# Kernel tuning notes

Hardware: AMD Instinct MI355X
Metric: run time of the kernel (lower is better)

## Reference

```python
import jax, jax.numpy as jnp
import numpy as np

ALPHA = 10.0   # args.alpha softmax sharpness
EPS = 1e-8     # torch CosineSimilarity eps


def setup_inputs() -> dict:
    key = jax.random.key(0)
    k0, k1, k2, k3 = jax.random.split(key, 4)
    B, S, F, D, C = 8, 1024, 32, 128, 16
    Hs = jax.random.normal(k0, (B, S, F, D), dtype=jnp.float32)
    Cj = jax.random.normal(k1, (C, D), dtype=jnp.float32)
    W = jax.random.normal(k2, (D, D), dtype=jnp.float32) * 0.05  # nn.Linear weight [out,in]
    b = jnp.zeros((D,), dtype=jnp.float32)
    importance = jax.random.uniform(k3, (B, S, F), dtype=jnp.float32)
    return {"Hs": Hs, "Cj": Cj, "W": W, "b": b, "importance": importance}


def reference(Hs, Cj, W, b, importance):
    # Hs: [B,S,F,D] features; Cj: [C,D] cluster centers; importance: [B,S,F]
    # Faithful to Model_DTSSOCC.assignment (importance is not None branch),
    # but avoids materializing the broadcasted [B,S,F,C,D] repeat tensors.
    Hn = Hs / jnp.maximum(jnp.linalg.norm(Hs, axis=-1, keepdims=True), EPS)
    Cn = Cj / jnp.maximum(jnp.linalg.norm(Cj, axis=-1, keepdims=True), EPS)
    cos = jnp.einsum('bsfd,cd->bsfc', Hn, Cn)            # cosine_sim4 over dim D
    logits = -ALPHA * 0.5 * (1.0 - cos)                  # -alpha * dists, [B,S,F,C]
    w3 = jax.nn.softmax(logits, axis=3)                  # softmax over centers
    w = jax.nn.softmax(logits, axis=2)                   # softmax over feas
    w3 = jnp.swapaxes(w3, 2, 3)                          # [B,S,C,F]
    w = jnp.swapaxes(w, 2, 3)                            # [B,S,C,F]
    F_tj = jax.nn.relu(jnp.einsum('bsfd,ed->bsfe', Hs, W) + b)  # relu(Linear(F_t))
    # importance update: bmm(w3, importance) then softmax over centers
    imp = jax.nn.softmax(jnp.einsum('bscf,bsf->bsc', w3, importance), axis=2)
    # weighted feature aggregation: bmm(w, F_tj) -> [B,S,C,D]
    f_t_new = jnp.einsum('bscf,bsfd->bscd', w, F_tj)
    return f_t_new, imp
```

## Files before the change

kernel.cpp:

```cpp
#include <hip/hip_runtime.h>
#include <hip/hip_bf16.h>
#include <math.h>

constexpr int Bn = 8, Sn = 1024, Fn = 32, Dn = 128, Cc = 16;
constexpr int NSITE = Bn * Sn;

#define EPSV 1e-8f

typedef __attribute__((ext_vector_type(8))) short bf16x8;
typedef __attribute__((ext_vector_type(4))) short bf16x4;
typedef __attribute__((ext_vector_type(4))) float f32x4;

__device__ inline short f2bf(float x) {
    __hip_bfloat16 h = __float2bfloat16(x);
    short s;
    __builtin_memcpy(&s, &h, sizeof(s));
    return s;
}

__device__ inline bf16x8 cvt8(f32x4 x0, f32x4 x1) {
    bf16x8 r;
    r[0] = f2bf(x0[0]); r[1] = f2bf(x0[1]); r[2] = f2bf(x0[2]); r[3] = f2bf(x0[3]);
    r[4] = f2bf(x1[0]); r[5] = f2bf(x1[1]); r[6] = f2bf(x1[2]); r[7] = f2bf(x1[3]);
    return r;
}

template<int CTRL>
__device__ __forceinline__ float dpp_add(float v) {
    union { float f; int i; } u, r;
    u.f = v;
    r.i = __builtin_amdgcn_update_dpp(0, u.i, CTRL, 0xf, 0xf, true);
    return v + r.f;
}
__device__ __forceinline__ float rowsum16(float v) {
    v = dpp_add<0x121>(v);
    v = dpp_add<0x122>(v);
    v = dpp_add<0x124>(v);
    v = dpp_add<0x128>(v);
    return v;
}
__device__ __forceinline__ float fastrcp(float x) { return __builtin_amdgcn_rcpf(x); }

__global__ void prep_kernel(const float* __restrict__ Cj,
                            const float* __restrict__ W,
                            short* __restrict__ CnPack,
                            short* __restrict__ Wb) {
    const int tid = threadIdx.x;
    if (blockIdx.x < 64) {
        int t = blockIdx.x * 256 + tid;
        int n = t >> 7, k = t & 127;
        short v = f2bf(W[n * Dn + k]);
        int frag = (n >> 4) * 4 + (k >> 5);
        int lane = ((k >> 3) & 3) * 16 + (n & 15);
        Wb[(frag * 64 + lane) * 8 + (k & 7)] = v;
    } else {
        int c = blockIdx.x - 64;
        __shared__ float part[2];
        float v = 0.f, sq = 0.f;
        if (tid < 128) {
            v = Cj[c * Dn + tid];
            sq = v * v;
            #pragma unroll
            for (int off = 32; off > 0; off >>= 1) sq += __shfl_down(sq, off);
        }
        if (tid < 128 && (tid & 63) == 0) part[tid >> 6] = sq;
        __syncthreads();
        if (tid < 128) {
            float cn = v / fmaxf(sqrtf(part[0] + part[1]), EPSV);
            int kt = tid >> 5, ln = ((tid >> 3) & 3) * 16 + c, j = tid & 7;
            CnPack[(kt * 64 + ln) * 8 + j] = f2bf(cn);
        }
    }
}

__launch_bounds__(64, 4)
__global__ void site_kernel(const float* __restrict__ Hs,
                            const short* __restrict__ CnPack,
                            const short* __restrict__ Wb,
                            const float* __restrict__ bvec,
                            const float* __restrict__ imp_in,
                            float* __restrict__ f_out,
                            float* __restrict__ imp_out) {
    __shared__ __align__(16) short F_tjT[128][40];
    __shared__ __align__(16) float sO[16][33];

    const int lane = threadIdx.x;
    const int c16  = lane & 15;
    const int g    = lane >> 4;
    const int site = blockIdx.x;

    const float* hsrc = Hs + (size_t)site * (Fn * Dn);
    const f32x4 zro = {0.f, 0.f, 0.f, 0.f};

    f32x4 x[16];
    #pragma unroll
    for (int kt = 0; kt < 4; ++kt) {
        const f32x4* p0 = (const f32x4*)(hsrc + c16 * Dn + kt * 32 + g * 8);
        const f32x4* p1 = (const f32x4*)(hsrc + (16 + c16) * Dn + kt * 32 + g * 8);
        x[4 * kt + 0] = p0[0];
        x[4 * kt + 1] = p0[1];
        x[4 * kt + 2] = p1[0];
        x[4 * kt + 3] = p1[1];
    }
    bf16x8 bcf[4];
    #pragma unroll
    for (int kt = 0; kt < 4; ++kt)
        bcf[kt] = *(const bf16x8*)&CnPack[(kt * 64 + lane) * 8];
    const float* impp = imp_in + (size_t)site * Fn;
    f32x4 impv0 = *(const f32x4*)(impp + 4 * g);
    f32x4 impv1 = *(const f32x4*)(impp + 16 + 4 * g);

    bf16x8 aF[2][4];
    #pragma unroll
    for (int kt = 0; kt < 4; ++kt) {
        aF[0][kt] = cvt8(x[4 * kt + 0], x[4 * kt + 1]);
        aF[1][kt] = cvt8(x[4 * kt + 2], x[4 * kt + 3]);
    }

    f32x4 gm0 = zro, gm1 = zro, cos0 = zro, cos1 = zro;
    #pragma unroll
    for (int kt = 0; kt < 4; ++kt) {
        gm0  = __builtin_amdgcn_mfma_f32_16x16x32_bf16(aF[0][kt], aF[0][kt], gm0, 0, 0, 0);
        gm1  = __builtin_amdgcn_mfma_f32_16x16x32_bf16(aF[1][kt], aF[1][kt], gm1, 0, 0, 0);
        cos0 = __builtin_amdgcn_mfma_f32_16x16x32_bf16(aF[0][kt], bcf[kt], cos0, 0, 0, 0);
        cos1 = __builtin_amdgcn_mfma_f32_16x16x32_bf16(aF[1][kt], bcf[kt], cos1, 0, 0, 0);
    }

    float e0[4], e1[4];
    #pragma unroll
    for (int r = 0; r < 4; ++r) {
        float q0 = __shfl(gm0[r], 20 * g + r);
        float q1 = __shfl(gm1[r], 20 * g + r);
        float i0 = fastrcp(fmaxf(sqrtf(q0), EPSV));
        float i1 = fastrcp(fmaxf(sqrtf(q1), EPSV));
        e0[r] = __expf(5.0f * cos0[r] * i0);
        e1[r] = __expf(5.0f * cos1[r] * i1);
    }

    bf16x8 wB;
    {
        float sum = 0.f;
        #pragma unroll
        for (int r = 0; r < 4; ++r) sum += e0[r] + e1[r];
        sum += __shfl_xor(sum, 16);
        sum += __shfl_xor(sum, 32);
        float inv = fastrcp(sum);
        const int srcA = c16 + 16 * ((2 * g) & 3);
        const int srcB = c16 + 16 * ((2 * g + 1) & 3);
        const bool hi = (g >= 2);
        #pragma unroll
        for (int r = 0; r < 4; ++r) {
            float a0 = __shfl(e0[r] * inv, srcA);
            float a1 = __shfl(e1[r] * inv, srcA);
            wB[r] = f2bf(hi ? a1 : a0);
            float b0 = __shfl(e0[r] * inv, srcB);
            float b1 = __shfl(e1[r] * inv, srcB);
            wB[4 + r] = f2bf(hi ? b1 : b0);
        }
    }

    {
        float t = 0.f;
        #pragma unroll
        for (int h = 0; h < 2; ++h) {
            #pragma unroll
            for (int r = 0; r < 4; ++r) {
                float e = h ? e1[r] : e0[r];
                float q3 = rowsum16(e);
                t += e * fastrcp(q3) * (h ? impv1[r] : impv0[r]);
            }
        }
        t += __shfl_xor(t, 16);
        t += __shfl_xor(t, 32);
        float ei = __expf(t);
        float si = rowsum16(ei);
        if (g == 0) imp_out[(size_t)site * Cc + c16] = ei * fastrcp(si);
    }

    #pragma unroll
    for (int nt = 0; nt < 8; ++nt) {
        bf16x8 bw0 = *(const bf16x8*)&Wb[((nt * 4) + 0) * 512 + lane * 8];
        bf16x8 bw1 = *(const bf16x8*)&Wb[((nt * 4) + 1) * 512 + lane * 8];
        bf16x8 bw2 = *(const bf16x8*)&Wb[((nt * 4) + 2) * 512 + lane * 8];
        bf16x8 bw3 = *(const bf16x8*)&Wb[((nt * 4) + 3) * 512 + lane * 8];
        f32x4 acc0 = zro, acc1 = zro;
        acc0 = __builtin_amdgcn_mfma_f32_16x16x32_bf16(aF[0][0], bw0, acc0, 0, 0, 0);
        acc1 = __builtin_amdgcn_mfma_f32_16x16x32_bf16(aF[1][0], bw0, acc1, 0, 0, 0);
        acc0 = __builtin_amdgcn_mfma_f32_16x16x32_bf16(aF[0][1], bw1, acc0, 0, 0, 0);
        acc1 = __builtin_amdgcn_mfma_f32_16x16x32_bf16(aF[1][1], bw1, acc1, 0, 0, 0);
        acc0 = __builtin_amdgcn_mfma_f32_16x16x32_bf16(aF[0][2], bw2, acc0, 0, 0, 0);
        acc1 = __builtin_amdgcn_mfma_f32_16x16x32_bf16(aF[1][2], bw2, acc1, 0, 0, 0);
        acc0 = __builtin_amdgcn_mfma_f32_16x16x32_bf16(aF[0][3], bw3, acc0, 0, 0, 0);
        acc1 = __builtin_amdgcn_mfma_f32_16x16x32_bf16(aF[1][3], bw3, acc1, 0, 0, 0);
        float bb = bvec[nt * 16 + c16];
        bf16x4 p0, p1;
        #pragma unroll
        for (int r = 0; r < 4; ++r) {
            p0[r] = f2bf(fmaxf(acc0[r] + bb, 0.f));
            p1[r] = f2bf(fmaxf(acc1[r] + bb, 0.f));
        }
        *(bf16x4*)&F_tjT[nt * 16 + c16][4 * g]      = p0;
        *(bf16x4*)&F_tjT[nt * 16 + c16][16 + 4 * g] = p1;
    }

    {
        float* op = f_out + (size_t)site * (Cc * Dn);
        #pragma unroll
        for (int p = 0; p < 4; ++p) {
            #pragma unroll
            for (int h = 0; h < 2; ++h) {
                const int nt = 2 * p + h;
                bf16x8 aFt = *(const bf16x8*)&F_tjT[nt * 16 + c16][8 * g];
                f32x4 o = __builtin_amdgcn_mfma_f32_16x16x32_bf16(aFt, wB, zro, 0, 0, 0);
                *(f32x4*)&sO[c16][h * 16 + 4 * g] = o;
            }
            #pragma unroll
            for (int i = 0; i < 2; ++i) {
                const int row = 8 * i + (lane >> 3);
                const int cir = lane & 7;
                f32x4 v = *(const f32x4*)&sO[row][cir * 4];
                *(f32x4*)(op + row * Dn + p * 32 + cir * 4) = v;
            }
        }
    }
}

extern "C" void kernel_launch(void* const* d_in, const int* in_sizes, int n_in,
                              void* d_out, int out_size, void* d_ws, size_t ws_size,
                              hipStream_t stream) {
    const float* Hs  = (const float*)d_in[0];
    const float* Cj  = (const float*)d_in[1];
    const float* W   = (const float*)d_in[2];
    const float* b   = (const float*)d_in[3];
    const float* imp = (const float*)d_in[4];

    float* f_out   = (float*)d_out;
    float* imp_out = f_out + (size_t)NSITE * Cc * Dn;

    short* CnPack = (short*)d_ws;
    short* Wb     = CnPack + Cc * Dn;

    hipLaunchKernelGGL(prep_kernel, dim3(80), dim3(256), 0, stream, Cj, W, CnPack, Wb);
    hipLaunchKernelGGL(site_kernel, dim3(NSITE), dim3(64), 0, stream,
                       Hs, CnPack, Wb, b, imp, f_out, imp_out);
}
```

Measured before the change: 44.63 us.

## Process two sites per wavefront with staggered loads of the second site

Each 64-thread block now handles two consecutive sites, launching half as many blocks. The second site's Hs loads are issued in two halves interleaved with the bf16 conversion of the first site, so more memory traffic is in flight per wave. The per-site compute is wrapped in a lambda and run sequentially for both sites. The extra register state for two sites is accommodated by lowering the launch-bounds occupancy hint from 4 to 3, which may reduce latency hiding across waves.

```diff
diff --git a/kernel.cpp b/kernel.cpp
--- a/kernel.cpp
+++ b/kernel.cpp
@@ -73,7 +73,7 @@
     }
 }
 
-__launch_bounds__(64, 4)
+__launch_bounds__(64, 3)
 __global__ void site_kernel(const float* __restrict__ Hs,
                             const short* __restrict__ CnPack,
                             const short* __restrict__ Wb,
@@ -87,142 +87,176 @@
     const int lane = threadIdx.x;
     const int c16  = lane & 15;
     const int g    = lane >> 4;
-    const int site = blockIdx.x;
-
-    const float* hsrc = Hs + (size_t)site * (Fn * Dn);
+    const int sA   = blockIdx.x * 2;
+    const int sB   = sA + 1;
+
+    const float* hA = Hs + (size_t)sA * (Fn * Dn);
+    const float* hB = Hs + (size_t)sB * (Fn * Dn);
     const f32x4 zro = {0.f, 0.f, 0.f, 0.f};
 
-    f32x4 x[16];
+    f32x4 xA[16], xB[16];
     #pragma unroll
     for (int kt = 0; kt < 4; ++kt) {
-        const f32x4* p0 = (const f32x4*)(hsrc + c16 * Dn + kt * 32 + g * 8);
-        const f32x4* p1 = (const f32x4*)(hsrc + (16 + c16) * Dn + kt * 32 + g * 8);
-        x[4 * kt + 0] = p0[0];
-        x[4 * kt + 1] = p0[1];
-        x[4 * kt + 2] = p1[0];
-        x[4 * kt + 3] = p1[1];
-    }
+        const f32x4* p0 = (const f32x4*)(hA + c16 * Dn + kt * 32 + g * 8);
+        const f32x4* p1 = (const f32x4*)(hA + (16 + c16) * Dn + kt * 32 + g * 8);
+        xA[4 * kt + 0] = p0[0];
+        xA[4 * kt + 1] = p0[1];
+        xA[4 * kt + 2] = p1[0];
+        xA[4 * kt + 3] = p1[1];
+    }
+    #pragma unroll
+    for (int kt = 0; kt < 2; ++kt) {
+        const f32x4* p0 = (const f32x4*)(hB + c16 * Dn + kt * 32 + g * 8);
+        const f32x4* p1 = (const f32x4*)(hB + (16 + c16) * Dn + kt * 32 + g * 8);
+        xB[4 * kt + 0] = p0[0];
+        xB[4 * kt + 1] = p0[1];
+        xB[4 * kt + 2] = p1[0];
+        xB[4 * kt + 3] = p1[1];
+    }
+    bf16x8 aFA[2][4], aFB[2][4];
+    #pragma unroll
+    for (int kt = 0; kt < 4; ++kt) {
+        aFA[0][kt] = cvt8(xA[4 * kt + 0], xA[4 * kt + 1]);
+        aFA[1][kt] = cvt8(xA[4 * kt + 2], xA[4 * kt + 3]);
+    }
+    #pragma unroll
+    for (int kt = 2; kt < 4; ++kt) {
+        const f32x4* p0 = (const f32x4*)(hB + c16 * Dn + kt * 32 + g * 8);
+        const f32x4* p1 = (const f32x4*)(hB + (16 + c16) * Dn + kt * 32 + g * 8);
+        xB[4 * kt + 0] = p0[0];
+        xB[4 * kt + 1] = p0[1];
+        xB[4 * kt + 2] = p1[0];
+        xB[4 * kt + 3] = p1[1];
+    }
+    #pragma unroll
+    for (int kt = 0; kt < 4; ++kt) {
+        aFB[0][kt] = cvt8(xB[4 * kt + 0], xB[4 * kt + 1]);
+        aFB[1][kt] = cvt8(xB[4 * kt + 2], xB[4 * kt + 3]);
+    }
+
     bf16x8 bcf[4];
     #pragma unroll
     for (int kt = 0; kt < 4; ++kt)
         bcf[kt] = *(const bf16x8*)&CnPack[(kt * 64 + lane) * 8];
-    const float* impp = imp_in + (size_t)site * Fn;
-    f32x4 impv0 = *(const f32x4*)(impp + 4 * g);
-    f32x4 impv1 = *(const f32x4*)(impp + 16 + 4 * g);
-
-    bf16x8 aF[2][4];
-    #pragma unroll
-    for (int kt = 0; kt < 4; ++kt) {
-        aF[0][kt] = cvt8(x[4 * kt + 0], x[4 * kt + 1]);
-        aF[1][kt] = cvt8(x[4 * kt + 2], x[4 * kt + 3]);
-    }
-
-    f32x4 gm0 = zro, gm1 = zro, cos0 = zro, cos1 = zro;
-    #pragma unroll
-    for (int kt = 0; kt < 4; ++kt) {
-        gm0  = __builtin_amdgcn_mfma_f32_16x16x32_bf16(aF[0][kt], aF[0][kt], gm0, 0, 0, 0);
-        gm1  = __builtin_amdgcn_mfma_f32_16x16x32_bf16(aF[1][kt], aF[1][kt], gm1, 0, 0, 0);
-        cos0 = __builtin_amdgcn_mfma_f32_16x16x32_bf16(aF[0][kt], bcf[kt], cos0, 0, 0, 0);
-        cos1 = __builtin_amdgcn_mfma_f32_16x16x32_bf16(aF[1][kt], bcf[kt], cos1, 0, 0, 0);
-    }
-
-    float e0[4], e1[4];
-    #pragma unroll
-    for (int r = 0; r < 4; ++r) {
-        float q0 = __shfl(gm0[r], 20 * g + r);
-        float q1 = __shfl(gm1[r], 20 * g + r);
-        float i0 = fastrcp(fmaxf(sqrtf(q0), EPSV));
-        float i1 = fastrcp(fmaxf(sqrtf(q1), EPSV));
-        e0[r] = __expf(5.0f * cos0[r] * i0);
-        e1[r] = __expf(5.0f * cos1[r] * i1);
-    }
-
-    bf16x8 wB;
-    {
-        float sum = 0.f;
+    const float* impA = imp_in + (size_t)sA * Fn;
+    const float* impB = imp_in + (size_t)sB * Fn;
+    f32x4 impA0 = *(const f32x4*)(impA + 4 * g);
+    f32x4 impA1 = *(const f32x4*)(impA + 16 + 4 * g);
+    f32x4 impB0 = *(const f32x4*)(impB + 4 * g);
+    f32x4 impB1 = *(const f32x4*)(impB + 16 + 4 * g);
+
+    auto run_site = [&](int site, const bf16x8 (&aF)[2][4],
+                        const f32x4& impv0, const f32x4& impv1) {
+        f32x4 gm0 = zro, gm1 = zro, cos0 = zro, cos1 = zro;
         #pragma unroll
-        for (int r = 0; r < 4; ++r) sum += e0[r] + e1[r];
-        sum += __shfl_xor(sum, 16);
-        sum += __shfl_xor(sum, 32);
-        float inv = fastrcp(sum);
-        const int srcA = c16 + 16 * ((2 * g) & 3);
-        const int srcB = c16 + 16 * ((2 * g + 1) & 3);
-        const bool hi = (g >= 2);
+        for (int kt = 0; kt < 4; ++kt) {
+            gm0  = __builtin_amdgcn_mfma_f32_16x16x32_bf16(aF[0][kt], aF[0][kt], gm0, 0, 0, 0);
+            gm1  = __builtin_amdgcn_mfma_f32_16x16x32_bf16(aF[1][kt], aF[1][kt], gm1, 0, 0, 0);
+            cos0 = __builtin_amdgcn_mfma_f32_16x16x32_bf16(aF[0][kt], bcf[kt], cos0, 0, 0, 0);
+            cos1 = __builtin_amdgcn_mfma_f32_16x16x32_bf16(aF[1][kt], bcf[kt], cos1, 0, 0, 0);
+        }
+
+        float e0[4], e1[4];
         #pragma unroll
         for (int r = 0; r < 4; ++r) {
-            float a0 = __shfl(e0[r] * inv, srcA);
-            float a1 = __shfl(e1[r] * inv, srcA);
-            wB[r] = f2bf(hi ? a1 : a0);
-            float b0 = __shfl(e0[r] * inv, srcB);
-            float b1 = __shfl(e1[r] * inv, srcB);
-            wB[4 + r] = f2bf(hi ? b1 : b0);
-        }
-    }
-
-    {
-        float t = 0.f;
+            float q0 = __shfl(gm0[r], 20 * g + r);
+            float q1 = __shfl(gm1[r], 20 * g + r);
+            float i0 = fastrcp(fmaxf(sqrtf(q0), EPSV));
+            float i1 = fastrcp(fmaxf(sqrtf(q1), EPSV));
+            e0[r] = __expf(5.0f * cos0[r] * i0);
+            e1[r] = __expf(5.0f * cos1[r] * i1);
+        }
+
+        bf16x8 wB;
+        {
+            float sum = 0.f;
+            #pragma unroll
+            for (int r = 0; r < 4; ++r) sum += e0[r] + e1[r];
+            sum += __shfl_xor(sum, 16);
+            sum += __shfl_xor(sum, 32);
+            float inv = fastrcp(sum);
+            const int srcA = c16 + 16 * ((2 * g) & 3);
+            const int srcB = c16 + 16 * ((2 * g + 1) & 3);
+            const bool hi = (g >= 2);
+            #pragma unroll
+            for (int r = 0; r < 4; ++r) {
+                float a0 = __shfl(e0[r] * inv, srcA);
+                float a1 = __shfl(e1[r] * inv, srcA);
+                wB[r] = f2bf(hi ? a1 : a0);
+                float b0 = __shfl(e0[r] * inv, srcB);
+                float b1 = __shfl(e1[r] * inv, srcB);
+                wB[4 + r] = f2bf(hi ? b1 : b0);
+            }
+        }
+
+        {
+            float t = 0.f;
+            #pragma unroll
+            for (int h = 0; h < 2; ++h) {
+                #pragma unroll
+                for (int r = 0; r < 4; ++r) {
+                    float e = h ? e1[r] : e0[r];
+                    float q3 = rowsum16(e);
+                    t += e * fastrcp(q3) * (h ? impv1[r] : impv0[r]);
+                }
+            }
+            t += __shfl_xor(t, 16);
+            t += __shfl_xor(t, 32);
+            float ei = __expf(t);
+            float si = rowsum16(ei);
+            if (g == 0) imp_out[(size_t)site * Cc + c16] = ei * fastrcp(si);
+        }
+
         #pragma unroll
-        for (int h = 0; h < 2; ++h) {
+        for (int nt = 0; nt < 8; ++nt) {
+            bf16x8 bw0 = *(const bf16x8*)&Wb[((nt * 4) + 0) * 512 + lane * 8];
+            bf16x8 bw1 = *(const bf16x8*)&Wb[((nt * 4) + 1) * 512 + lane * 8];
+            bf16x8 bw2 = *(const bf16x8*)&Wb[((nt * 4) + 2) * 512 + lane * 8];
+            bf16x8 bw3 = *(const bf16x8*)&Wb[((nt * 4) + 3) * 512 + lane * 8];
+            f32x4 acc0 = zro, acc1 = zro;
+            acc0 = __builtin_amdgcn_mfma_f32_16x16x32_bf16(aF[0][0], bw0, acc0, 0, 0, 0);
+            acc1 = __builtin_amdgcn_mfma_f32_16x16x32_bf16(aF[1][0], bw0, acc1, 0, 0, 0);
+            acc0 = __builtin_amdgcn_mfma_f32_16x16x32_bf16(aF[0][1], bw1, acc0, 0, 0, 0);
+            acc1 = __builtin_amdgcn_mfma_f32_16x16x32_bf16(aF[1][1], bw1, acc1, 0, 0, 0);
+            acc0 = __builtin_amdgcn_mfma_f32_16x16x32_bf16(aF[0][2], bw2, acc0, 0, 0, 0);
+            acc1 = __builtin_amdgcn_mfma_f32_16x16x32_bf16(aF[1][2], bw2, acc1, 0, 0, 0);
+            acc0 = __builtin_amdgcn_mfma_f32_16x16x32_bf16(aF[0][3], bw3, acc0, 0, 0, 0);
+            acc1 = __builtin_amdgcn_mfma_f32_16x16x32_bf16(aF[1][3], bw3, acc1, 0, 0, 0);
+            float bb = bvec[nt * 16 + c16];
+            bf16x4 p0, p1;
             #pragma unroll
             for (int r = 0; r < 4; ++r) {
-                float e = h ? e1[r] : e0[r];
-                float q3 = rowsum16(e);
-                t += e * fastrcp(q3) * (h ? impv1[r] : impv0[r]);
-            }
-        }
-        t += __shfl_xor(t, 16);
-        t += __shfl_xor(t, 32);
-        float ei = __expf(t);
-        float si = rowsum16(ei);
-        if (g == 0) imp_out[(size_t)site * Cc + c16] = ei * fastrcp(si);
-    }
-
-    #pragma unroll
-    for (int nt = 0; nt < 8; ++nt) {
-        bf16x8 bw0 = *(const bf16x8*)&Wb[((nt * 4) + 0) * 512 + lane * 8];
-        bf16x8 bw1 = *(const bf16x8*)&Wb[((nt * 4) + 1) * 512 + lane * 8];
-        bf16x8 bw2 = *(const bf16x8*)&Wb[((nt * 4) + 2) * 512 + lane * 8];
-        bf16x8 bw3 = *(const bf16x8*)&Wb[((nt * 4) + 3) * 512 + lane * 8];
-        f32x4 acc0 = zro, acc1 = zro;
-        acc0 = __builtin_amdgcn_mfma_f32_16x16x32_bf16(aF[0][0], bw0, acc0, 0, 0, 0);
-        acc1 = __builtin_amdgcn_mfma_f32_16x16x32_bf16(aF[1][0], bw0, acc1, 0, 0, 0);
-        acc0 = __builtin_amdgcn_mfma_f32_16x16x32_bf16(aF[0][1], bw1, acc0, 0, 0, 0);
-        acc1 = __builtin_amdgcn_mfma_f32_16x16x32_bf16(aF[1][1], bw1, acc1, 0, 0, 0);
-        acc0 = __builtin_amdgcn_mfma_f32_16x16x32_bf16(aF[0][2], bw2, acc0, 0, 0, 0);
-        acc1 = __builtin_amdgcn_mfma_f32_16x16x32_bf16(aF[1][2], bw2, acc1, 0, 0, 0);
-        acc0 = __builtin_amdgcn_mfma_f32_16x16x32_bf16(aF[0][3], bw3, acc0, 0, 0, 0);
-        acc1 = __builtin_amdgcn_mfma_f32_16x16x32_bf16(aF[1][3], bw3, acc1, 0, 0, 0);
-        float bb = bvec[nt * 16 + c16];
-        bf16x4 p0, p1;
-        #pragma unroll
-        for (int r = 0; r < 4; ++r) {
-            p0[r] = f2bf(fmaxf(acc0[r] + bb, 0.f));
-            p1[r] = f2bf(fmaxf(acc1[r] + bb, 0.f));
-        }
-        *(bf16x4*)&F_tjT[nt * 16 + c16][4 * g]      = p0;
-        *(bf16x4*)&F_tjT[nt * 16 + c16][16 + 4 * g] = p1;
-    }
-
-    {
-        float* op = f_out + (size_t)site * (Cc * Dn);
-        #pragma unroll
-        for (int p = 0; p < 4; ++p) {
-            #pragma unroll
-            for (int h = 0; h < 2; ++h) {
-                const int nt = 2 * p + h;
-                bf16x8 aFt = *(const bf16x8*)&F_tjT[nt * 16 + c16][8 * g];
-                f32x4 o = __builtin_amdgcn_mfma_f32_16x16x32_bf16(aFt, wB, zro, 0, 0, 0);
-                *(f32x4*)&sO[c16][h * 16 + 4 * g] = o;
-            }
-            #pragma unroll
-            for (int i = 0; i < 2; ++i) {
-                const int row = 8 * i + (lane >> 3);
-                const int cir = lane & 7;
-                f32x4 v = *(const f32x4*)&sO[row][cir * 4];
-                *(f32x4*)(op + row * Dn + p * 32 + cir * 4) = v;
-            }
-        }
-    }
+                p0[r] = f2bf(fmaxf(acc0[r] + bb, 0.f));
+                p1[r] = f2bf(fmaxf(acc1[r] + bb, 0.f));
+            }
+            *(bf16x4*)&F_tjT[nt * 16 + c16][4 * g]      = p0;
+            *(bf16x4*)&F_tjT[nt * 16 + c16][16 + 4 * g] = p1;
+        }
+
+        {
+            float* op = f_out + (size_t)site * (Cc * Dn);
+            #pragma unroll
+            for (int p = 0; p < 4; ++p) {
+                #pragma unroll
+                for (int h = 0; h < 2; ++h) {
+                    const int nt = 2 * p + h;
+                    bf16x8 aFt = *(const bf16x8*)&F_tjT[nt * 16 + c16][8 * g];
+                    f32x4 o = __builtin_amdgcn_mfma_f32_16x16x32_bf16(aFt, wB, zro, 0, 0, 0);
+                    *(f32x4*)&sO[c16][h * 16 + 4 * g] = o;
+                }
+                #pragma unroll
+                for (int i = 0; i < 2; ++i) {
+                    const int row = 8 * i + (lane >> 3);
+                    const int cir = lane & 7;
+                    f32x4 v = *(const f32x4*)&sO[row][cir * 4];
+                    *(f32x4*)(op + row * Dn + p * 32 + cir * 4) = v;
+                }
+            }
+        }
+    };
+
+    run_site(sA, aFA, impA0, impA1);
+    run_site(sB, aFB, impB0, impB1);
 }
 
 extern "C" void kernel_launch(void* const* d_in, const int* in_sizes, int n_in,
@@ -241,6 +275,6 @@
     short* Wb     = CnPack + Cc * Dn;
 
     hipLaunchKernelGGL(prep_kernel, dim3(80), dim3(256), 0, stream, Cj, W, CnPack, Wb);
-    hipLaunchKernelGGL(site_kernel, dim3(NSITE), dim3(64), 0, stream,
+    hipLaunchKernelGGL(site_kernel, dim3(NSITE / 2), dim3(64), 0, stream,
                        Hs, CnPack, Wb, b, imp, f_out, imp_out);
 }
```

After: 52.19 us. 16.9% more time.

## Fuse weight and center prep into site kernel, dropping the prep launch

Applied to the files above, without the earlier changes.

Removes the separate prep kernel that packed W and normalized Cj into bf16 fragment layouts. Each site block now loads Cj and W directly as fp32, converts them to bf16 in registers, and computes center norms with an extra MFMA Gram product. This saves a kernel launch and the serialization before the main kernel. In exchange every block reads twice as many bytes of W and does redundant conversion and norm work, across 8192 blocks.

```diff
diff --git a/kernel.cpp b/kernel.cpp
--- a/kernel.cpp
+++ b/kernel.cpp
@@ -41,42 +41,10 @@
 }
 __device__ __forceinline__ float fastrcp(float x) { return __builtin_amdgcn_rcpf(x); }
 
-__global__ void prep_kernel(const float* __restrict__ Cj,
-                            const float* __restrict__ W,
-                            short* __restrict__ CnPack,
-                            short* __restrict__ Wb) {
-    const int tid = threadIdx.x;
-    if (blockIdx.x < 64) {
-        int t = blockIdx.x * 256 + tid;
-        int n = t >> 7, k = t & 127;
-        short v = f2bf(W[n * Dn + k]);
-        int frag = (n >> 4) * 4 + (k >> 5);
-        int lane = ((k >> 3) & 3) * 16 + (n & 15);
-        Wb[(frag * 64 + lane) * 8 + (k & 7)] = v;
-    } else {
-        int c = blockIdx.x - 64;
-        __shared__ float part[2];
-        float v = 0.f, sq = 0.f;
-        if (tid < 128) {
-            v = Cj[c * Dn + tid];
-            sq = v * v;
-            #pragma unroll
-            for (int off = 32; off > 0; off >>= 1) sq += __shfl_down(sq, off);
-        }
-        if (tid < 128 && (tid & 63) == 0) part[tid >> 6] = sq;
-        __syncthreads();
-        if (tid < 128) {
-            float cn = v / fmaxf(sqrtf(part[0] + part[1]), EPSV);
-            int kt = tid >> 5, ln = ((tid >> 3) & 3) * 16 + c, j = tid & 7;
-            CnPack[(kt * 64 + ln) * 8 + j] = f2bf(cn);
-        }
-    }
-}
-
 __launch_bounds__(64, 4)
 __global__ void site_kernel(const float* __restrict__ Hs,
-                            const short* __restrict__ CnPack,
-                            const short* __restrict__ Wb,
+                            const float* __restrict__ Cj,
+                            const float* __restrict__ W,
                             const float* __restrict__ bvec,
                             const float* __restrict__ imp_in,
                             float* __restrict__ f_out,
@@ -104,8 +72,10 @@
     }
     bf16x8 bcf[4];
     #pragma unroll
-    for (int kt = 0; kt < 4; ++kt)
-        bcf[kt] = *(const bf16x8*)&CnPack[(kt * 64 + lane) * 8];
+    for (int kt = 0; kt < 4; ++kt) {
+        const f32x4* cp = (const f32x4*)(Cj + c16 * Dn + kt * 32 + g * 8);
+        bcf[kt] = cvt8(cp[0], cp[1]);
+    }
     const float* impp = imp_in + (size_t)site * Fn;
     f32x4 impv0 = *(const f32x4*)(impp + 4 * g);
     f32x4 impv1 = *(const f32x4*)(impp + 16 + 4 * g);
@@ -117,13 +87,22 @@
         aF[1][kt] = cvt8(x[4 * kt + 2], x[4 * kt + 3]);
     }
 
-    f32x4 gm0 = zro, gm1 = zro, cos0 = zro, cos1 = zro;
+    f32x4 gm0 = zro, gm1 = zro, gmC = zro, cos0 = zro, cos1 = zro;
     #pragma unroll
     for (int kt = 0; kt < 4; ++kt) {
         gm0  = __builtin_amdgcn_mfma_f32_16x16x32_bf16(aF[0][kt], aF[0][kt], gm0, 0, 0, 0);
         gm1  = __builtin_amdgcn_mfma_f32_16x16x32_bf16(aF[1][kt], aF[1][kt], gm1, 0, 0, 0);
+        gmC  = __builtin_amdgcn_mfma_f32_16x16x32_bf16(bcf[kt], bcf[kt], gmC, 0, 0, 0);
         cos0 = __builtin_amdgcn_mfma_f32_16x16x32_bf16(aF[0][kt], bcf[kt], cos0, 0, 0, 0);
         cos1 = __builtin_amdgcn_mfma_f32_16x16x32_bf16(aF[1][kt], bcf[kt], cos1, 0, 0, 0);
+    }
+
+    float invC;
+    {
+        float sel = (c16 & 2) ? ((c16 & 1) ? gmC[3] : gmC[2])
+                              : ((c16 & 1) ? gmC[1] : gmC[0]);
+        float q = __shfl(sel, 16 * (c16 >> 2) + c16);
+        invC = fastrcp(fmaxf(sqrtf(q), EPSV));
     }
 
     float e0[4], e1[4];
@@ -133,8 +112,8 @@
         float q1 = __shfl(gm1[r], 20 * g + r);
         float i0 = fastrcp(fmaxf(sqrtf(q0), EPSV));
         float i1 = fastrcp(fmaxf(sqrtf(q1), EPSV));
-        e0[r] = __expf(5.0f * cos0[r] * i0);
-        e1[r] = __expf(5.0f * cos1[r] * i1);
+        e0[r] = __expf(5.0f * cos0[r] * i0 * invC);
+        e1[r] = __expf(5.0f * cos1[r] * i1 * invC);
     }
 
     bf16x8 wB;
@@ -179,10 +158,15 @@
 
     #pragma unroll
     for (int nt = 0; nt < 8; ++nt) {
-        bf16x8 bw0 = *(const bf16x8*)&Wb[((nt * 4) + 0) * 512 + lane * 8];
-        bf16x8 bw1 = *(const bf16x8*)&Wb[((nt * 4) + 1) * 512 + lane * 8];
-        bf16x8 bw2 = *(const bf16x8*)&Wb[((nt * 4) + 2) * 512 + lane * 8];
-        bf16x8 bw3 = *(const bf16x8*)&Wb[((nt * 4) + 3) * 512 + lane * 8];
+        const float* wp = W + (size_t)(nt * 16 + c16) * Dn + g * 8;
+        const f32x4* w0 = (const f32x4*)(wp);
+        const f32x4* w1 = (const f32x4*)(wp + 32);
+        const f32x4* w2 = (const f32x4*)(wp + 64);
+        const f32x4* w3 = (const f32x4*)(wp + 96);
+        bf16x8 bw0 = cvt8(w0[0], w0[1]);
+        bf16x8 bw1 = cvt8(w1[0], w1[1]);
+        bf16x8 bw2 = cvt8(w2[0], w2[1]);
+        bf16x8 bw3 = cvt8(w3[0], w3[1]);
         f32x4 acc0 = zro, acc1 = zro;
         acc0 = __builtin_amdgcn_mfma_f32_16x16x32_bf16(aF[0][0], bw0, acc0, 0, 0, 0);
         acc1 = __builtin_amdgcn_mfma_f32_16x16x32_bf16(aF[1][0], bw0, acc1, 0, 0, 0);
@@ -237,10 +221,6 @@
     float* f_out   = (float*)d_out;
     float* imp_out = f_out + (size_t)NSITE * Cc * Dn;
 
-    short* CnPack = (short*)d_ws;
-    short* Wb     = CnPack + Cc * Dn;
-
-    hipLaunchKernelGGL(prep_kernel, dim3(80), dim3(256), 0, stream, Cj, W, CnPack, Wb);
     hipLaunchKernelGGL(site_kernel, dim3(NSITE), dim3(64), 0, stream,
-                       Hs, CnPack, Wb, b, imp, f_out, imp_out);
-}
+                       Hs, Cj, W, b, imp, f_out, imp_out);
+}
```

Result: slower. 100.4 us (+124.9%).
